# Performance work log

Measured on AMD Instinct MI355X. Metric: run time of the kernel, lower is better.

Reference implementation:

```python
import jax, jax.numpy as jnp
import numpy as np
from functools import partial

H = 1024  # hidden_sz
B, T = 32, 256
NL = 4    # stacked LSTM layers
WSCALE = 0.02


def setup_inputs() -> dict:
    key = jax.random.key(0)
    ks = jax.random.split(key, 8)
    x = jax.random.normal(ks[0], (B, T, H), dtype=jnp.float32)
    h0 = jnp.zeros((B, H), dtype=jnp.float32)
    c0 = jnp.zeros((B, H), dtype=jnp.float32)
    # LSTM params per layer: kernel [H,4H], recurrent kernel [H,4H], bias [4H]
    Wk = jax.random.normal(ks[1], (NL, H, 4 * H), dtype=jnp.float32) * WSCALE
    Wr = jax.random.normal(ks[2], (NL, H, 4 * H), dtype=jnp.float32) * WSCALE
    b = jnp.zeros((NL, 4 * H), dtype=jnp.float32)
    # dense head
    Wd = jax.random.normal(ks[3], (H, H), dtype=jnp.float32) * WSCALE
    bd = jnp.zeros((H,), dtype=jnp.float32)
    return {"x": x, "h0": h0, "c0": c0, "Wk": Wk, "Wr": Wr, "b": b, "Wd": Wd, "bd": bd}


def _lstm_layer(x_tbd, h0, c0, Wk, Wr, b):
    # Keras LSTM with activation='relu', recurrent_activation='sigmoid'.
    # Gate order in keras kernels: i, f, c(candidate), o.
    xw = jnp.einsum('tbd,dg->tbg', x_tbd, Wk) + b  # precompute input projections [T,B,4H]

    def step(carry, xw_t):
        h, c = carry
        z = xw_t + h @ Wr  # [B,4H]
        i, f, g, o = jnp.split(z, 4, axis=-1)
        i = jax.nn.sigmoid(i)
        f = jax.nn.sigmoid(f)
        o = jax.nn.sigmoid(o)
        c = f * c + i * jax.nn.relu(g)
        h = o * jax.nn.relu(c)
        return (h, c), h

    (hT, cT), hs = jax.lax.scan(step, (h0, c0), xw)
    return hs, hT, cT  # hs: [T,B,H]


def reference(x, h0, c0, Wk, Wr, b, Wd, bd):
    # x: [B,T,H] -> time-major [T,B,H]
    seq = jnp.transpose(x, (1, 0, 2))
    h, c = h0, c0
    for l in range(NL):
        seq, h, c = _lstm_layer(seq, h, c, Wk[l], Wr[l], b[l])
        # dropout layers are identity at inference (training=False)
    out = jnp.einsum('tbh,hd->tbd', seq, Wd) + bd
    out = jnp.transpose(out, (1, 0, 2))  # back to [B,T,H]
    return out, h, c
```

## Files before the change

### kernel.cpp

```cpp
#include <hip/hip_runtime.h>

#define TT 256
#define BB 32
#define HH 1024
#define GG 4096

typedef __attribute__((ext_vector_type(8))) short short8;
typedef __attribute__((ext_vector_type(4))) float f32x4;

__device__ __forceinline__ unsigned short rne_bf16(float x) {
    unsigned u = __float_as_uint(x);
    unsigned r = (u + 0x7FFFu + ((u >> 16) & 1u)) >> 16;
    return (unsigned short)r;
}
__device__ __forceinline__ float bf16f(unsigned short s) {
    return __uint_as_float((unsigned)s << 16);
}

__global__ __launch_bounds__(256) void k_transpose(const float* __restrict__ x, float* __restrict__ seq) {
    int idx = blockIdx.x * 256 + threadIdx.x;
    int k4 = idx & 255;
    int tb = idx >> 8;
    int t = tb >> 5, b = tb & 31;
    float4 v = ((const float4*)x)[((size_t)b * TT + t) * 256 + k4];
    ((float4*)seq)[(size_t)tb * 256 + k4] = v;
}

__global__ __launch_bounds__(256) void k_init_hc(const float* __restrict__ h0, const float* __restrict__ c0,
                                                 float* __restrict__ h, float* __restrict__ c) {
    int i = blockIdx.x * 256 + threadIdx.x;
    ((float4*)h)[i] = ((const float4*)h0)[i];
    ((float4*)c)[i] = ((const float4*)c0)[i];
}

__global__ __launch_bounds__(256) void k_init_hc2(const float* __restrict__ h0, const float* __restrict__ c0,
                                                  float* __restrict__ h, float* __restrict__ c,
                                                  unsigned short* __restrict__ hb1,
                                                  unsigned short* __restrict__ hb2,
                                                  unsigned short* __restrict__ hb3) {
    int i = blockIdx.x * 256 + threadIdx.x;
    float4 hv = ((const float4*)h0)[i];
    ((float4*)h)[i] = hv;
    ((float4*)c)[i] = ((const float4*)c0)[i];
    float xs[4] = {hv.x, hv.y, hv.z, hv.w};
    ushort4 o1, o2, o3;
    unsigned short* p1 = (unsigned short*)&o1;
    unsigned short* p2 = (unsigned short*)&o2;
    unsigned short* p3 = (unsigned short*)&o3;
#pragma unroll
    for (int e = 0; e < 4; ++e) {
        unsigned short s1 = rne_bf16(xs[e]);
        float r1 = xs[e] - bf16f(s1);
        unsigned short s2 = rne_bf16(r1);
        float r2 = r1 - bf16f(s2);
        p1[e] = s1; p2[e] = s2; p3[e] = rne_bf16(r2);
    }
    *(ushort4*)&hb1[i * 4] = o1;
    *(ushort4*)&hb2[i * 4] = o2;
    *(ushort4*)&hb3[i * 4] = o3;
}

__global__ __launch_bounds__(256) void k_copy_hc(const float* __restrict__ h, const float* __restrict__ c,
                                                 float* __restrict__ oh, float* __restrict__ oc) {
    int i = blockIdx.x * 256 + threadIdx.x;
    ((float4*)oh)[i] = ((const float4*)h)[i];
    ((float4*)oc)[i] = ((const float4*)c)[i];
}

__global__ __launch_bounds__(256) void k_wrt(const float* __restrict__ Wr, float* __restrict__ WrT) {
    __shared__ float tile[64][65];
    int c0 = blockIdx.x * 64;
    int k0 = blockIdx.y * 64;
    int tid = threadIdx.x;
    int tr = tid >> 4, tc4 = tid & 15;
#pragma unroll
    for (int p = 0; p < 4; ++p) {
        int r = p * 16 + tr;
        float4 v = *(const float4*)&Wr[(size_t)(k0 + r) * GG + c0 + tc4 * 4];
        tile[r][tc4 * 4 + 0] = v.x;
        tile[r][tc4 * 4 + 1] = v.y;
        tile[r][tc4 * 4 + 2] = v.z;
        tile[r][tc4 * 4 + 3] = v.w;
    }
    __syncthreads();
#pragma unroll
    for (int p = 0; p < 4; ++p) {
        int cc = p * 16 + tr;
        float4 v;
        v.x = tile[tc4 * 4 + 0][cc];
        v.y = tile[tc4 * 4 + 1][cc];
        v.z = tile[tc4 * 4 + 2][cc];
        v.w = tile[tc4 * 4 + 3][cc];
        *(float4*)&WrT[(size_t)(c0 + cc) * 1024 + k0 + tc4 * 4] = v;
    }
}

__global__ __launch_bounds__(256) void k_wrt3(const float* __restrict__ Wr, unsigned short* __restrict__ W1,
                                              unsigned short* __restrict__ W2, unsigned short* __restrict__ W3) {
    __shared__ float tile[64][65];
    int c0 = blockIdx.x * 64;
    int k0 = blockIdx.y * 64;
    int tid = threadIdx.x;
    int tr = tid >> 4, tc4 = tid & 15;
#pragma unroll
    for (int p = 0; p < 4; ++p) {
        int r = p * 16 + tr;
        float4 v = *(const float4*)&Wr[(size_t)(k0 + r) * GG + c0 + tc4 * 4];
        tile[r][tc4 * 4 + 0] = v.x;
        tile[r][tc4 * 4 + 1] = v.y;
        tile[r][tc4 * 4 + 2] = v.z;
        tile[r][tc4 * 4 + 3] = v.w;
    }
    __syncthreads();
    int cc = tid & 63, kq = tid >> 6;
    int G = c0 + cc;
    int outrow = ((G & 1023) >> 2) * 16 + (G >> 10) * 4 + (G & 3);
    size_t obase = (size_t)outrow * 1024 + k0 + kq * 16;
    unsigned short t1[16], t2[16], t3[16];
#pragma unroll
    for (int e = 0; e < 16; ++e) {
        float v = tile[kq * 16 + e][cc];
        unsigned short s1 = rne_bf16(v);
        float r1 = v - bf16f(s1);
        unsigned short s2 = rne_bf16(r1);
        float r2 = r1 - bf16f(s2);
        t1[e] = s1; t2[e] = s2; t3[e] = rne_bf16(r2);
    }
#pragma unroll
    for (int hlf = 0; hlf < 2; ++hlf) {
        *(short8*)&W1[obase + hlf * 8] = *(short8*)&t1[hlf * 8];
        *(short8*)&W2[obase + hlf * 8] = *(short8*)&t2[hlf * 8];
        *(short8*)&W3[obase + hlf * 8] = *(short8*)&t3[hlf * 8];
    }
}

__global__ __launch_bounds__(256) void k_wkt3(const float* __restrict__ Wk, unsigned short* __restrict__ W1,
                                              unsigned short* __restrict__ W2, unsigned short* __restrict__ W3) {
    __shared__ float tile[64][65];
    int c0 = blockIdx.x * 64;
    int k0 = blockIdx.y * 64;
    int tid = threadIdx.x;
    int tr = tid >> 4, tc4 = tid & 15;
#pragma unroll
    for (int p = 0; p < 4; ++p) {
        int r = p * 16 + tr;
        float4 v = *(const float4*)&Wk[(size_t)(k0 + r) * GG + c0 + tc4 * 4];
        tile[r][tc4 * 4 + 0] = v.x;
        tile[r][tc4 * 4 + 1] = v.y;
        tile[r][tc4 * 4 + 2] = v.z;
        tile[r][tc4 * 4 + 3] = v.w;
    }
    __syncthreads();
#pragma unroll
    for (int p = 0; p < 4; ++p) {
        int cc = p * 16 + tr;
        ushort4 o1, o2, o3;
        unsigned short* po1 = (unsigned short*)&o1;
        unsigned short* po2 = (unsigned short*)&o2;
        unsigned short* po3 = (unsigned short*)&o3;
#pragma unroll
        for (int e = 0; e < 4; ++e) {
            float v = tile[tc4 * 4 + e][cc];
            unsigned short s1 = rne_bf16(v);
            float r1 = v - bf16f(s1);
            unsigned short s2 = rne_bf16(r1);
            float r2 = r1 - bf16f(s2);
            po1[e] = s1; po2[e] = s2; po3[e] = rne_bf16(r2);
        }
        size_t off = (size_t)(c0 + cc) * 1024 + k0 + tc4 * 4;
        *(ushort4*)&W1[off] = o1;
        *(ushort4*)&W2[off] = o2;
        *(ushort4*)&W3[off] = o3;
    }
}

__global__ __launch_bounds__(256, 2) void k_gemm_mx3(const float* __restrict__ A,
                                                     const unsigned short* __restrict__ B1,
                                                     const unsigned short* __restrict__ B2,
                                                     const unsigned short* __restrict__ B3,
                                                     const float* __restrict__ bias, float* __restrict__ C) {
    __shared__ unsigned short Asl[3][6144];
    __shared__ unsigned short Bsl[3][6144];
    int tid = threadIdx.x;
    int m0 = blockIdx.x * 128, n0 = blockIdx.y * 128;
    int lane = tid & 63, wv = tid >> 6;
    int wr = (wv >> 1) * 64, wc = (wv & 1) * 64;
    int l15 = lane & 15, ko = (lane >> 4) * 8;

    f32x4 acc[4][4];
#pragma unroll
    for (int i = 0; i < 4; ++i)
#pragma unroll
        for (int j = 0; j < 4; ++j) acc[i][j] = (f32x4){0.f, 0.f, 0.f, 0.f};

    const unsigned short* Bg[3] = {B1, B2, B3};

    for (int k0 = 0; k0 < 1024; k0 += 32) {
#pragma unroll
        for (int i = 0; i < 4; ++i) {
            int idx = i * 256 + tid;
            int m = idx >> 3, kq = idx & 7;
            float4 v = *(const float4*)&A[(size_t)(m0 + m) * 1024 + k0 + kq * 4];
            float xs[4] = {v.x, v.y, v.z, v.w};
            ushort4 o1, o2, o3;
            unsigned short* po1 = (unsigned short*)&o1;
            unsigned short* po2 = (unsigned short*)&o2;
            unsigned short* po3 = (unsigned short*)&o3;
#pragma unroll
            for (int e = 0; e < 4; ++e) {
                unsigned short s1 = rne_bf16(xs[e]);
                float r1 = xs[e] - bf16f(s1);
                unsigned short s2 = rne_bf16(r1);
                float r2 = r1 - bf16f(s2);
                po1[e] = s1; po2[e] = s2; po3[e] = rne_bf16(r2);
            }
            int loff = m * 48 + kq * 4;
            *(ushort4*)&Asl[0][loff] = o1;
            *(ushort4*)&Asl[1][loff] = o2;
            *(ushort4*)&Asl[2][loff] = o3;
        }
#pragma unroll
        for (int sp = 0; sp < 3; ++sp) {
            const unsigned short* bg = Bg[sp];
#pragma unroll
            for (int i = 0; i < 2; ++i) {
                int idx = i * 256 + tid;
                int n = idx >> 2, kq = idx & 3;
                short8 v = *(const short8*)&bg[(size_t)(n0 + n) * 1024 + k0 + kq * 8];
                *(short8*)&Bsl[sp][n * 48 + kq * 8] = v;
            }
        }
        __syncthreads();

        short8 af[3][4];
#pragma unroll
        for (int mi = 0; mi < 4; ++mi) {
            int ro = (wr + mi * 16 + l15) * 48 + ko;
#pragma unroll
            for (int sp = 0; sp < 3; ++sp) af[sp][mi] = *(const short8*)&Asl[sp][ro];
        }
#pragma unroll
        for (int ni = 0; ni < 4; ++ni) {
            int co = (wc + ni * 16 + l15) * 48 + ko;
            short8 b0 = *(const short8*)&Bsl[0][co];
            short8 b1 = *(const short8*)&Bsl[1][co];
            short8 b2 = *(const short8*)&Bsl[2][co];
#pragma unroll
            for (int mi = 0; mi < 4; ++mi) {
                f32x4 a = acc[mi][ni];
                a = __builtin_amdgcn_mfma_f32_16x16x32_bf16(af[0][mi], b0, a, 0, 0, 0);
                a = __builtin_amdgcn_mfma_f32_16x16x32_bf16(af[1][mi], b0, a, 0, 0, 0);
                a = __builtin_amdgcn_mfma_f32_16x16x32_bf16(af[0][mi], b1, a, 0, 0, 0);
                a = __builtin_amdgcn_mfma_f32_16x16x32_bf16(af[2][mi], b0, a, 0, 0, 0);
                a = __builtin_amdgcn_mfma_f32_16x16x32_bf16(af[1][mi], b1, a, 0, 0, 0);
                a = __builtin_amdgcn_mfma_f32_16x16x32_bf16(af[0][mi], b2, a, 0, 0, 0);
                acc[mi][ni] = a;
            }
        }
        __syncthreads();
    }

#pragma unroll
    for (int ni = 0; ni < 4; ++ni) {
        int col = n0 + wc + ni * 16 + l15;
        float bv = bias[col];
#pragma unroll
        for (int mi = 0; mi < 4; ++mi) {
            int rbase = m0 + wr + mi * 16 + (lane >> 4) * 4;
#pragma unroll
            for (int r = 0; r < 4; ++r)
                C[(size_t)(rbase + r) * 4096 + col] = acc[mi][ni][r] + bv;
        }
    }
}

template <int MODE>
__global__ __launch_bounds__(256) void k_gemm(const float* __restrict__ A, const float* __restrict__ W,
                                              const float* __restrict__ bias, float* __restrict__ C, int N) {
    __shared__ float As[16][132];
    __shared__ float Bs[16][132];
    const int K = 1024;
    int tid = threadIdx.x;
    int m0 = blockIdx.x * 128, n0 = blockIdx.y * 128;
    int tx = tid & 15, ty = tid >> 4;
    int a_row = tid >> 2, a_kq = tid & 3;
    int b_cq = tid & 31, b_k = tid >> 5;
    float acc[8][8];
#pragma unroll
    for (int i = 0; i < 8; ++i)
#pragma unroll
        for (int jj = 0; jj < 8; ++jj) acc[i][jj] = 0.f;

    for (int kc = 0; kc < K; kc += 16) {
#pragma unroll
        for (int it = 0; it < 2; ++it) {
            int row = a_row + it * 64;
            float4 v = *(const float4*)&A[(size_t)(m0 + row) * K + kc + a_kq * 4];
            As[a_kq * 4 + 0][row] = v.x;
            As[a_kq * 4 + 1][row] = v.y;
            As[a_kq * 4 + 2][row] = v.z;
            As[a_kq * 4 + 3][row] = v.w;
        }
#pragma unroll
        for (int it = 0; it < 2; ++it) {
            int kk = b_k + it * 8;
            float4 v = *(const float4*)&W[(size_t)(kc + kk) * N + n0 + b_cq * 4];
            *(float4*)&Bs[kk][b_cq * 4] = v;
        }
        __syncthreads();
#pragma unroll
        for (int kk = 0; kk < 16; ++kk) {
            float4 a0 = *(const float4*)&As[kk][ty * 8];
            float4 a1 = *(const float4*)&As[kk][ty * 8 + 4];
            float4 b0 = *(const float4*)&Bs[kk][tx * 8];
            float4 b1 = *(const float4*)&Bs[kk][tx * 8 + 4];
            float am[8] = {a0.x, a0.y, a0.z, a0.w, a1.x, a1.y, a1.z, a1.w};
            float bv[8] = {b0.x, b0.y, b0.z, b0.w, b1.x, b1.y, b1.z, b1.w};
#pragma unroll
            for (int i = 0; i < 8; ++i)
#pragma unroll
                for (int jj = 0; jj < 8; ++jj) acc[i][jj] += am[i] * bv[jj];
        }
        __syncthreads();
    }
#pragma unroll
    for (int i = 0; i < 8; ++i) {
        int m = m0 + ty * 8 + i;
#pragma unroll
        for (int jj = 0; jj < 8; jj += 4) {
            int n = n0 + tx * 8 + jj;
            float4 v;
            v.x = acc[i][jj + 0] + bias[n + 0];
            v.y = acc[i][jj + 1] + bias[n + 1];
            v.z = acc[i][jj + 2] + bias[n + 2];
            v.w = acc[i][jj + 3] + bias[n + 3];
            if (MODE == 0) {
                *(float4*)&C[(size_t)m * N + n] = v;
            } else {
                int t = m >> 5, b = m & 31;
                *(float4*)&C[((size_t)b * TT + t) * HH + n] = v;
            }
        }
    }
}

__global__ __launch_bounds__(512) void k_step_mfma(
    const unsigned short* __restrict__ Wb1, const unsigned short* __restrict__ Wb2,
    const unsigned short* __restrict__ Wb3,
    const unsigned short* __restrict__ Ha1, const unsigned short* __restrict__ Ha2,
    const unsigned short* __restrict__ Ha3,
    unsigned short* __restrict__ Ho1, unsigned short* __restrict__ Ho2,
    unsigned short* __restrict__ Ho3,
    const float* __restrict__ xw_t, float* __restrict__ seq_t,
    float* __restrict__ h_out, float* __restrict__ c) {
    __shared__ float zs[8][16][33];
    int tid = threadIdx.x;
    int lane = tid & 63, wv = tid >> 6;
    int blk = blockIdx.x;
    int l15 = lane & 15, ko = (lane >> 4) * 8;

    int rb = tid >> 2, rd = tid & 3;
    float pz[4];
    if (tid < 128) {
#pragma unroll
        for (int g = 0; g < 4; ++g) pz[g] = xw_t[rb * GG + g * HH + blk * 4 + rd];
    }

    size_t bbase  = ((size_t)blk * 16 + l15) * 1024 + ko;
    size_t abase0 = (size_t)l15 * 1024 + ko;
    size_t abase1 = (size_t)(16 + l15) * 1024 + ko;

    f32x4 acc0 = (f32x4){0.f, 0.f, 0.f, 0.f};
    f32x4 acc1 = (f32x4){0.f, 0.f, 0.f, 0.f};

#pragma unroll
    for (int kt = 0; kt < 4; ++kt) {
        int kk = (wv * 4 + kt) * 32;
        short8 b0  = *(const short8*)&Wb1[bbase + kk];
        short8 b1  = *(const short8*)&Wb2[bbase + kk];
        short8 b2  = *(const short8*)&Wb3[bbase + kk];
        short8 a00 = *(const short8*)&Ha1[abase0 + kk];
        short8 a01 = *(const short8*)&Ha2[abase0 + kk];
        short8 a02 = *(const short8*)&Ha3[abase0 + kk];
        short8 a10 = *(const short8*)&Ha1[abase1 + kk];
        short8 a11 = *(const short8*)&Ha2[abase1 + kk];
        short8 a12 = *(const short8*)&Ha3[abase1 + kk];
        acc0 = __builtin_amdgcn_mfma_f32_16x16x32_bf16(a00, b0, acc0, 0, 0, 0);
        acc0 = __builtin_amdgcn_mfma_f32_16x16x32_bf16(a01, b0, acc0, 0, 0, 0);
        acc0 = __builtin_amdgcn_mfma_f32_16x16x32_bf16(a00, b1, acc0, 0, 0, 0);
        acc0 = __builtin_amdgcn_mfma_f32_16x16x32_bf16(a02, b0, acc0, 0, 0, 0);
        acc0 = __builtin_amdgcn_mfma_f32_16x16x32_bf16(a01, b1, acc0, 0, 0, 0);
        acc0 = __builtin_amdgcn_mfma_f32_16x16x32_bf16(a00, b2, acc0, 0, 0, 0);
        acc1 = __builtin_amdgcn_mfma_f32_16x16x32_bf16(a10, b0, acc1, 0, 0, 0);
        acc1 = __builtin_amdgcn_mfma_f32_16x16x32_bf16(a11, b0, acc1, 0, 0, 0);
        acc1 = __builtin_amdgcn_mfma_f32_16x16x32_bf16(a10, b1, acc1, 0, 0, 0);
        acc1 = __builtin_amdgcn_mfma_f32_16x16x32_bf16(a12, b0, acc1, 0, 0, 0);
        acc1 = __builtin_amdgcn_mfma_f32_16x16x32_bf16(a11, b1, acc1, 0, 0, 0);
        acc1 = __builtin_amdgcn_mfma_f32_16x16x32_bf16(a10, b2, acc1, 0, 0, 0);
    }

#pragma unroll
    for (int r = 0; r < 4; ++r) {
        zs[wv][l15][(lane >> 4) * 4 + r]      = acc0[r];
        zs[wv][l15][16 + (lane >> 4) * 4 + r] = acc1[r];
    }
    __syncthreads();

    if (tid < 128) {
        float zz[4];
#pragma unroll
        for (int g = 0; g < 4; ++g) {
            float s = pz[g];
#pragma unroll
            for (int u = 0; u < 8; ++u) s += zs[u][g * 4 + rd][rb];
            zz[g] = s;
        }
        float si = 1.f / (1.f + expf(-zz[0]));
        float sf = 1.f / (1.f + expf(-zz[1]));
        float gg = fmaxf(zz[2], 0.f);
        float so = 1.f / (1.f + expf(-zz[3]));
        int hi = rb * HH + blk * 4 + rd;
        float cv = c[hi];
        cv = sf * cv + si * gg;
        c[hi] = cv;
        float hn = so * fmaxf(cv, 0.f);
        h_out[hi] = hn;
        seq_t[hi] = hn;
        unsigned short s1 = rne_bf16(hn);
        float r1 = hn - bf16f(s1);
        unsigned short s2 = rne_bf16(r1);
        float r2 = r1 - bf16f(s2);
        Ho1[hi] = s1; Ho2[hi] = s2; Ho3[hi] = rne_bf16(r2);
    }
}

__global__ __launch_bounds__(512) void k_step_T3(const float* __restrict__ WrT, const float* __restrict__ xw_t,
                                                 float* __restrict__ seq_t, const float* __restrict__ h_in,
                                                 float* __restrict__ h_out, float* __restrict__ c) {
    __shared__ float h_lds[34816];
    __shared__ float zred[8][32][17];
    int tid = threadIdx.x;
    int j = tid & 15, ks = tid >> 4;
    int hc0 = blockIdx.x * 4;
    int col = (j >> 2) * HH + hc0 + (j & 3);

    const float4* WrT4 = (const float4*)WrT;
    int wbase = col * 256 + ks * 8;
    float4 w[8];
#pragma unroll
    for (int q = 0; q < 8; ++q) w[q] = WrT4[wbase + q];

    int rb = tid >> 2, rd = tid & 3;
    float pz[4];
    if (tid < 128) {
#pragma unroll
        for (int g = 0; g < 4; ++g) pz[g] = xw_t[rb * GG + g * HH + hc0 + rd];
    }

    const float4* hp4 = (const float4*)h_in;
    float4* hl4w = (float4*)h_lds;
#pragma unroll 8
    for (int it = 0; it < 16; ++it) {
        int gi = it * 512 + tid;
        float4 v = hp4[gi];
        int b = gi >> 8, kk = gi & 255;
        hl4w[b * 272 + (kk >> 4) * 17 + (kk & 15)] = v;
    }
    __syncthreads();

    const float4* hl4 = (const float4*)h_lds;
    int base4 = (ks >> 1) * 17 + (ks & 1) * 8;
    float acc[32];
#pragma unroll
    for (int b = 0; b < 32; ++b) acc[b] = 0.f;
#pragma unroll
    for (int q = 0; q < 8; ++q) {
        float4 wq = w[q];
#pragma unroll
        for (int b = 0; b < 32; ++b) {
            float4 hv = hl4[b * 272 + base4 + q];
            acc[b] += wq.x * hv.x + wq.y * hv.y + wq.z * hv.z + wq.w * hv.w;
        }
    }
#pragma unroll
    for (int b = 0; b < 32; ++b) {
        acc[b] += __shfl_xor(acc[b], 16);
        acc[b] += __shfl_xor(acc[b], 32);
    }
    int wv = tid >> 6;
    if ((ks & 3) == 0) {
#pragma unroll
        for (int b = 0; b < 32; ++b) zred[wv][b][j] = acc[b];
    }
    __syncthreads();

    if (tid < 128) {
        float zz[4];
#pragma unroll
        for (int g = 0; g < 4; ++g) {
            float s = pz[g];
#pragma unroll
            for (int u = 0; u < 8; ++u) s += zred[u][rb][g * 4 + rd];
            zz[g] = s;
        }
        float si = 1.f / (1.f + expf(-zz[0]));
        float sf = 1.f / (1.f + expf(-zz[1]));
        float gg = fmaxf(zz[2], 0.f);
        float so = 1.f / (1.f + expf(-zz[3]));
        float cv = c[rb * HH + hc0 + rd];
        cv = sf * cv + si * gg;
        c[rb * HH + hc0 + rd] = cv;
        float hn = so * fmaxf(cv, 0.f);
        h_out[rb * HH + hc0 + rd] = hn;
        seq_t[rb * HH + hc0 + rd] = hn;
    }
}

__global__ __launch_bounds__(256) void k_step(const float* __restrict__ Wr, const float* __restrict__ xw_t,
                                              float* __restrict__ seq_t, const float* __restrict__ h_in,
                                              float* __restrict__ h_out, float* __restrict__ c) {
    __shared__ float zred[4][32][17];
    int tid = threadIdx.x;
    int j = tid & 15, ks = tid >> 4;
    int hc0 = blockIdx.x * 4;
    int col = (j >> 2) * HH + hc0 + (j & 3);
    float4 w[16];
#pragma unroll
    for (int q = 0; q < 16; ++q) {
        size_t kb = (size_t)(ks * 64 + q * 4) * GG + col;
        w[q].x = Wr[kb];
        w[q].y = Wr[kb + GG];
        w[q].z = Wr[kb + 2 * (size_t)GG];
        w[q].w = Wr[kb + 3 * (size_t)GG];
    }
    const float4* hp = (const float4*)h_in;
    int kq0 = ks * 16;
    float acc[32];
#pragma unroll
    for (int b = 0; b < 32; ++b) acc[b] = 0.f;
#pragma unroll
    for (int q = 0; q < 16; ++q) {
        float4 wq = w[q];
#pragma unroll
        for (int b = 0; b < 32; ++b) {
            float4 hv = hp[b * 256 + kq0 + q];
            acc[b] += wq.x * hv.x + wq.y * hv.y + wq.z * hv.z + wq.w * hv.w;
        }
    }
#pragma unroll
    for (int b = 0; b < 32; ++b) {
        acc[b] += __shfl_xor(acc[b], 16);
        acc[b] += __shfl_xor(acc[b], 32);
    }
    int wv = tid >> 6;
    if ((ks & 3) == 0) {
#pragma unroll
        for (int b = 0; b < 32; ++b) zred[wv][b][j] = acc[b];
    }
    __syncthreads();
    if (tid < 128) {
        int rb = tid >> 2, rd = tid & 3;
        float zz[4];
#pragma unroll
        for (int g = 0; g < 4; ++g) {
            float s = xw_t[rb * GG + g * HH + hc0 + rd];
#pragma unroll
            for (int u = 0; u < 4; ++u) s += zred[u][rb][g * 4 + rd];
            zz[g] = s;
        }
        float si = 1.f / (1.f + expf(-zz[0]));
        float sf = 1.f / (1.f + expf(-zz[1]));
        float gg = fmaxf(zz[2], 0.f);
        float so = 1.f / (1.f + expf(-zz[3]));
        float cv = c[rb * HH + hc0 + rd];
        cv = sf * cv + si * gg;
        c[rb * HH + hc0 + rd] = cv;
        float hn = so * fmaxf(cv, 0.f);
        h_out[rb * HH + hc0 + rd] = hn;
        seq_t[rb * HH + hc0 + rd] = hn;
    }
}

extern "C" void kernel_launch(void* const* d_in, const int* in_sizes, int n_in,
                              void* d_out, int out_size, void* d_ws, size_t ws_size,
                              hipStream_t stream) {
    const float* x  = (const float*)d_in[0];
    const float* h0 = (const float*)d_in[1];
    const float* c0 = (const float*)d_in[2];
    const float* Wk = (const float*)d_in[3];
    const float* Wr = (const float*)d_in[4];
    const float* bs = (const float*)d_in[5];
    const float* Wd = (const float*)d_in[6];
    const float* bd = (const float*)d_in[7];
    float* out = (float*)d_out;
    float* ws  = (float*)d_ws;

    float* xw  = ws;
    float* seq = ws + 33554432;
    float* h0b = seq + 8388608;
    float* h1b = h0b + 32768;
    float* c   = h1b + 32768;
    float* wrt = c + 32768;
    const size_t base_floats = 46235648;
    unsigned short* wkt1 = (unsigned short*)(ws + base_floats);
    unsigned short* wkt2 = wkt1 + 4194304;
    unsigned short* wkt3 = wkt2 + 4194304;
    unsigned short* wrb1 = wkt3 + 4194304;
    unsigned short* wrb2 = wrb1 + 4194304;
    unsigned short* wrb3 = wrb2 + 4194304;
    unsigned short* hA1  = wrb3 + 4194304;
    unsigned short* hA2  = hA1 + 32768;
    unsigned short* hA3  = hA2 + 32768;
    unsigned short* hB1  = hA3 + 32768;
    unsigned short* hB2  = hB1 + 32768;
    unsigned short* hB3  = hB2 + 32768;

    bool fast     = ws_size >= base_floats * 4;
    bool mfma_ok  = ws_size >= base_floats * 4 + (size_t)3 * 4194304 * 2;
    bool mfma2_ok = ws_size >= base_floats * 4 + (size_t)6 * 4194304 * 2 + 6 * 32768 * 2;

    k_transpose<<<8192, 256, 0, stream>>>(x, seq);
    if (mfma2_ok)
        k_init_hc2<<<32, 256, 0, stream>>>(h0, c0, h0b, c, hA1, hA2, hA3);
    else
        k_init_hc<<<32, 256, 0, stream>>>(h0, c0, h0b, c);

    for (int l = 0; l < 4; ++l) {
        const float* Wrl = Wr + (size_t)l * 1024 * 4096;
        const float* Wkl = Wk + (size_t)l * 1024 * 4096;
        if (mfma_ok) {
            k_wkt3<<<dim3(64, 16), 256, 0, stream>>>(Wkl, wkt1, wkt2, wkt3);
            k_gemm_mx3<<<dim3(64, 32), 256, 0, stream>>>(seq, wkt1, wkt2, wkt3, bs + l * 4096, xw);
        } else {
            k_gemm<0><<<dim3(64, 32), 256, 0, stream>>>(seq, Wkl, bs + l * 4096, xw, 4096);
        }
        if (mfma2_ok) {
            k_wrt3<<<dim3(64, 16), 256, 0, stream>>>(Wrl, wrb1, wrb2, wrb3);
            for (int t = 0; t < TT; ++t) {
                float* hout = (t & 1) ? h0b : h1b;
                const unsigned short* i1 = (t & 1) ? hB1 : hA1;
                const unsigned short* i2 = (t & 1) ? hB2 : hA2;
                const unsigned short* i3 = (t & 1) ? hB3 : hA3;
                unsigned short* o1 = (t & 1) ? hA1 : hB1;
                unsigned short* o2 = (t & 1) ? hA2 : hB2;
                unsigned short* o3 = (t & 1) ? hA3 : hB3;
                k_step_mfma<<<256, 512, 0, stream>>>(wrb1, wrb2, wrb3, i1, i2, i3, o1, o2, o3,
                                                     xw + (size_t)t * (BB * GG),
                                                     seq + (size_t)t * (BB * HH), hout, c);
            }
        } else {
            if (fast) k_wrt<<<dim3(64, 16), 256, 0, stream>>>(Wrl, wrt);
            for (int t = 0; t < TT; ++t) {
                const float* hin = (t & 1) ? h1b : h0b;
                float* hout      = (t & 1) ? h0b : h1b;
                if (fast)
                    k_step_T3<<<256, 512, 0, stream>>>(wrt, xw + (size_t)t * (BB * GG),
                                                       seq + (size_t)t * (BB * HH), hin, hout, c);
                else
                    k_step<<<256, 256, 0, stream>>>(Wrl, xw + (size_t)t * (BB * GG),
                                                    seq + (size_t)t * (BB * HH), hin, hout, c);
            }
        }
    }

    k_gemm<1><<<dim3(64, 8), 256, 0, stream>>>(seq, Wd, bd, out, 1024);
    k_copy_hc<<<32, 256, 0, stream>>>(h0b, c, out + 8388608, out + 8388608 + 32768);
}
```

Before: 13.48 ms.

## Store layer outputs as pre-split bf16 triples and use MFMA for dense head

The step kernel now writes each new hidden state directly as three bf16 split components, and the input-projection GEMM consumes these pre-split activations, so it no longer re-splits fp32 activations inside the GEMM. The final dense head also moves from the fp32 fallback GEMM to the split-bf16 MFMA GEMM, with Wd pre-transposed and split. This path is gated on a larger workspace. It trades extra bf16 storage and more global stores per step for less conversion work and matrix-core use in the dense head.

```diff
diff --git a/kernel.cpp b/kernel.cpp
--- a/kernel.cpp
+++ b/kernel.cpp
@@ -15,6 +15,34 @@
 }
 __device__ __forceinline__ float bf16f(unsigned short s) {
     return __uint_as_float((unsigned)s << 16);
+}
+
+__global__ __launch_bounds__(256) void k_transpose3(const float* __restrict__ x,
+                                                    unsigned short* __restrict__ s1,
+                                                    unsigned short* __restrict__ s2,
+                                                    unsigned short* __restrict__ s3) {
+    int idx = blockIdx.x * 256 + threadIdx.x;
+    int k4 = idx & 255;
+    int tb = idx >> 8;
+    int t = tb >> 5, b = tb & 31;
+    float4 v = ((const float4*)x)[((size_t)b * TT + t) * 256 + k4];
+    float xs[4] = {v.x, v.y, v.z, v.w};
+    ushort4 o1, o2, o3;
+    unsigned short* p1 = (unsigned short*)&o1;
+    unsigned short* p2 = (unsigned short*)&o2;
+    unsigned short* p3 = (unsigned short*)&o3;
+#pragma unroll
+    for (int e = 0; e < 4; ++e) {
+        unsigned short q1 = rne_bf16(xs[e]);
+        float r1 = xs[e] - bf16f(q1);
+        unsigned short q2 = rne_bf16(r1);
+        float r2 = r1 - bf16f(q2);
+        p1[e] = q1; p2[e] = q2; p3[e] = rne_bf16(r2);
+    }
+    size_t off = (size_t)tb * HH + k4 * 4;
+    *(ushort4*)&s1[off] = o1;
+    *(ushort4*)&s2[off] = o2;
+    *(ushort4*)&s3[off] = o3;
 }
 
 __global__ __launch_bounds__(256) void k_transpose(const float* __restrict__ x, float* __restrict__ seq) {
@@ -134,8 +162,10 @@
     }
 }
 
-__global__ __launch_bounds__(256) void k_wkt3(const float* __restrict__ Wk, unsigned short* __restrict__ W1,
-                                              unsigned short* __restrict__ W2, unsigned short* __restrict__ W3) {
+__global__ __launch_bounds__(256) void k_wt3(const float* __restrict__ W, int N,
+                                             unsigned short* __restrict__ W1,
+                                             unsigned short* __restrict__ W2,
+                                             unsigned short* __restrict__ W3) {
     __shared__ float tile[64][65];
     int c0 = blockIdx.x * 64;
     int k0 = blockIdx.y * 64;
@@ -144,7 +174,7 @@
 #pragma unroll
     for (int p = 0; p < 4; ++p) {
         int r = p * 16 + tr;
-        float4 v = *(const float4*)&Wk[(size_t)(k0 + r) * GG + c0 + tc4 * 4];
+        float4 v = *(const float4*)&W[(size_t)(k0 + r) * N + c0 + tc4 * 4];
         tile[r][tc4 * 4 + 0] = v.x;
         tile[r][tc4 * 4 + 1] = v.y;
         tile[r][tc4 * 4 + 2] = v.z;
@@ -171,6 +201,95 @@
         *(ushort4*)&W1[off] = o1;
         *(ushort4*)&W2[off] = o2;
         *(ushort4*)&W3[off] = o3;
+    }
+}
+
+template <int MODE>
+__global__ __launch_bounds__(256, 2) void k_gemm_mx3s(const unsigned short* __restrict__ A1,
+                                                      const unsigned short* __restrict__ A2,
+                                                      const unsigned short* __restrict__ A3,
+                                                      const unsigned short* __restrict__ B1,
+                                                      const unsigned short* __restrict__ B2,
+                                                      const unsigned short* __restrict__ B3,
+                                                      const float* __restrict__ bias, float* __restrict__ C) {
+    __shared__ unsigned short Asl[3][6144];
+    __shared__ unsigned short Bsl[3][6144];
+    int tid = threadIdx.x;
+    int m0 = blockIdx.x * 128, n0 = blockIdx.y * 128;
+    int lane = tid & 63, wv = tid >> 6;
+    int wr = (wv >> 1) * 64, wc = (wv & 1) * 64;
+    int l15 = lane & 15, ko = (lane >> 4) * 8;
+
+    f32x4 acc[4][4];
+#pragma unroll
+    for (int i = 0; i < 4; ++i)
+#pragma unroll
+        for (int j = 0; j < 4; ++j) acc[i][j] = (f32x4){0.f, 0.f, 0.f, 0.f};
+
+    const unsigned short* Ag[3] = {A1, A2, A3};
+    const unsigned short* Bg[3] = {B1, B2, B3};
+
+    for (int k0 = 0; k0 < 1024; k0 += 32) {
+#pragma unroll
+        for (int sp = 0; sp < 3; ++sp) {
+#pragma unroll
+            for (int i = 0; i < 2; ++i) {
+                int idx = i * 256 + tid;
+                int r = idx >> 2, kq = idx & 3;
+                short8 va = *(const short8*)&Ag[sp][(size_t)(m0 + r) * 1024 + k0 + kq * 8];
+                *(short8*)&Asl[sp][r * 48 + kq * 8] = va;
+                short8 vb = *(const short8*)&Bg[sp][(size_t)(n0 + r) * 1024 + k0 + kq * 8];
+                *(short8*)&Bsl[sp][r * 48 + kq * 8] = vb;
+            }
+        }
+        __syncthreads();
+
+        short8 af[3][4];
+#pragma unroll
+        for (int mi = 0; mi < 4; ++mi) {
+            int ro = (wr + mi * 16 + l15) * 48 + ko;
+#pragma unroll
+            for (int sp = 0; sp < 3; ++sp) af[sp][mi] = *(const short8*)&Asl[sp][ro];
+        }
+#pragma unroll
+        for (int ni = 0; ni < 4; ++ni) {
+            int co = (wc + ni * 16 + l15) * 48 + ko;
+            short8 b0 = *(const short8*)&Bsl[0][co];
+            short8 b1 = *(const short8*)&Bsl[1][co];
+            short8 b2 = *(const short8*)&Bsl[2][co];
+#pragma unroll
+            for (int mi = 0; mi < 4; ++mi) {
+                f32x4 a = acc[mi][ni];
+                a = __builtin_amdgcn_mfma_f32_16x16x32_bf16(af[0][mi], b0, a, 0, 0, 0);
+                a = __builtin_amdgcn_mfma_f32_16x16x32_bf16(af[1][mi], b0, a, 0, 0, 0);
+                a = __builtin_amdgcn_mfma_f32_16x16x32_bf16(af[0][mi], b1, a, 0, 0, 0);
+                a = __builtin_amdgcn_mfma_f32_16x16x32_bf16(af[2][mi], b0, a, 0, 0, 0);
+                a = __builtin_amdgcn_mfma_f32_16x16x32_bf16(af[1][mi], b1, a, 0, 0, 0);
+                a = __builtin_amdgcn_mfma_f32_16x16x32_bf16(af[0][mi], b2, a, 0, 0, 0);
+                acc[mi][ni] = a;
+            }
+        }
+        __syncthreads();
+    }
+
+#pragma unroll
+    for (int ni = 0; ni < 4; ++ni) {
+        int col = n0 + wc + ni * 16 + l15;
+        float bv = bias[col];
+#pragma unroll
+        for (int mi = 0; mi < 4; ++mi) {
+            int rbase = m0 + wr + mi * 16 + (lane >> 4) * 4;
+#pragma unroll
+            for (int r = 0; r < 4; ++r) {
+                int m = rbase + r;
+                if (MODE == 0) {
+                    C[(size_t)m * 4096 + col] = acc[mi][ni][r] + bv;
+                } else {
+                    int t = m >> 5, b = m & 31;
+                    C[((size_t)b * TT + t) * HH + col] = acc[mi][ni][r] + bv;
+                }
+            }
+        }
     }
 }
 
@@ -351,7 +470,9 @@
     const unsigned short* __restrict__ Ha3,
     unsigned short* __restrict__ Ho1, unsigned short* __restrict__ Ho2,
     unsigned short* __restrict__ Ho3,
-    const float* __restrict__ xw_t, float* __restrict__ seq_t,
+    const float* __restrict__ xw_t,
+    unsigned short* __restrict__ sq1, unsigned short* __restrict__ sq2,
+    unsigned short* __restrict__ sq3, float* __restrict__ seq_t,
     float* __restrict__ h_out, float* __restrict__ c) {
     __shared__ float zs[8][16][33];
     int tid = threadIdx.x;
@@ -425,12 +546,17 @@
         c[hi] = cv;
         float hn = so * fmaxf(cv, 0.f);
         h_out[hi] = hn;
-        seq_t[hi] = hn;
         unsigned short s1 = rne_bf16(hn);
         float r1 = hn - bf16f(s1);
         unsigned short s2 = rne_bf16(r1);
         float r2 = r1 - bf16f(s2);
-        Ho1[hi] = s1; Ho2[hi] = s2; Ho3[hi] = rne_bf16(r2);
+        unsigned short s3 = rne_bf16(r2);
+        Ho1[hi] = s1; Ho2[hi] = s2; Ho3[hi] = s3;
+        if (sq1) {
+            sq1[hi] = s1; sq2[hi] = s2; sq3[hi] = s3;
+        } else {
+            seq_t[hi] = hn;
+        }
     }
 }
 
@@ -614,22 +740,38 @@
     unsigned short* hB1  = hA3 + 32768;
     unsigned short* hB2  = hB1 + 32768;
     unsigned short* hB3  = hB2 + 32768;
-
+    unsigned short* sq1  = (unsigned short*)seq;
+    unsigned short* sq2  = sq1 + 8388608;
+    unsigned short* sq3  = hB3 + 32768;
+
+    const size_t mfma2_floats = base_floats + ((size_t)6 * 4194304 * 2 + 6 * 32768 * 2 + 3) / 4;
+    const size_t mfma3_floats = mfma2_floats + ((size_t)8388608 * 2 + 3) / 4;
     bool fast     = ws_size >= base_floats * 4;
-    bool mfma_ok  = ws_size >= base_floats * 4 + (size_t)3 * 4194304 * 2;
-    bool mfma2_ok = ws_size >= base_floats * 4 + (size_t)6 * 4194304 * 2 + 6 * 32768 * 2;
-
-    k_transpose<<<8192, 256, 0, stream>>>(x, seq);
-    if (mfma2_ok)
+    bool mfma_ok  = ws_size >= (base_floats + (size_t)3 * 4194304 / 2 * 4) ;
+    bool mfma2_ok = ws_size >= mfma2_floats * 4;
+    bool mfma3_ok = ws_size >= mfma3_floats * 4;
+    mfma_ok = ws_size >= base_floats * 4 + (size_t)3 * 4194304 * 2;
+
+    if (mfma3_ok) {
+        k_transpose3<<<8192, 256, 0, stream>>>(x, sq1, sq2, sq3);
         k_init_hc2<<<32, 256, 0, stream>>>(h0, c0, h0b, c, hA1, hA2, hA3);
-    else
-        k_init_hc<<<32, 256, 0, stream>>>(h0, c0, h0b, c);
+    } else {
+        k_transpose<<<8192, 256, 0, stream>>>(x, seq);
+        if (mfma2_ok)
+            k_init_hc2<<<32, 256, 0, stream>>>(h0, c0, h0b, c, hA1, hA2, hA3);
+        else
+            k_init_hc<<<32, 256, 0, stream>>>(h0, c0, h0b, c);
+    }
 
     for (int l = 0; l < 4; ++l) {
         const float* Wrl = Wr + (size_t)l * 1024 * 4096;
         const float* Wkl = Wk + (size_t)l * 1024 * 4096;
-        if (mfma_ok) {
-            k_wkt3<<<dim3(64, 16), 256, 0, stream>>>(Wkl, wkt1, wkt2, wkt3);
+        if (mfma3_ok) {
+            k_wt3<<<dim3(64, 16), 256, 0, stream>>>(Wkl, 4096, wkt1, wkt2, wkt3);
+            k_gemm_mx3s<0><<<dim3(64, 32), 256, 0, stream>>>(sq1, sq2, sq3, wkt1, wkt2, wkt3,
+                                                             bs + l * 4096, xw);
+        } else if (mfma_ok) {
+            k_wt3<<<dim3(64, 16), 256, 0, stream>>>(Wkl, 4096, wkt1, wkt2, wkt3);
             k_gemm_mx3<<<dim3(64, 32), 256, 0, stream>>>(seq, wkt1, wkt2, wkt3, bs + l * 4096, xw);
         } else {
             k_gemm<0><<<dim3(64, 32), 256, 0, stream>>>(seq, Wkl, bs + l * 4096, xw, 4096);
@@ -644,9 +786,18 @@
                 unsigned short* o1 = (t & 1) ? hA1 : hB1;
                 unsigned short* o2 = (t & 1) ? hA2 : hB2;
                 unsigned short* o3 = (t & 1) ? hA3 : hB3;
-                k_step_mfma<<<256, 512, 0, stream>>>(wrb1, wrb2, wrb3, i1, i2, i3, o1, o2, o3,
-                                                     xw + (size_t)t * (BB * GG),
-                                                     seq + (size_t)t * (BB * HH), hout, c);
+                if (mfma3_ok)
+                    k_step_mfma<<<256, 512, 0, stream>>>(wrb1, wrb2, wrb3, i1, i2, i3, o1, o2, o3,
+                                                         xw + (size_t)t * (BB * GG),
+                                                         sq1 + (size_t)t * (BB * HH),
+                                                         sq2 + (size_t)t * (BB * HH),
+                                                         sq3 + (size_t)t * (BB * HH),
+                                                         nullptr, hout, c);
+                else
+                    k_step_mfma<<<256, 512, 0, stream>>>(wrb1, wrb2, wrb3, i1, i2, i3, o1, o2, o3,
+                                                         xw + (size_t)t * (BB * GG),
+                                                         nullptr, nullptr, nullptr,
+                                                         seq + (size_t)t * (BB * HH), hout, c);
             }
         } else {
             if (fast) k_wrt<<<dim3(64, 16), 256, 0, stream>>>(Wrl, wrt);
@@ -663,6 +814,11 @@
         }
     }
 
-    k_gemm<1><<<dim3(64, 8), 256, 0, stream>>>(seq, Wd, bd, out, 1024);
+    if (mfma3_ok) {
+        k_wt3<<<dim3(16, 16), 256, 0, stream>>>(Wd, 1024, wkt1, wkt2, wkt3);
+        k_gemm_mx3s<1><<<dim3(64, 8), 256, 0, stream>>>(sq1, sq2, sq3, wkt1, wkt2, wkt3, bd, out);
+    } else {
+        k_gemm<1><<<dim3(64, 8), 256, 0, stream>>>(seq, Wd, bd, out, 1024);
+    }
     k_copy_hc<<<32, 256, 0, stream>>>(h0b, c, out + 8388608, out + 8388608 + 32768);
 }
```

Measured after the change: 13.54 ms. Within noise of the previous version (+0.5%).
